# Optimization experiments

Hardware: AMD Instinct MI355X
Metric: run time of the kernel (lower is better)

## Reference

```python
import jax, jax.numpy as jnp
import numpy as np


def _mlp(h, weights, biases, n_relu):
    # Linear(+ReLU) stack; ReLU on the first n_relu layers, final layer linear only.
    for i, (w, b) in enumerate(zip(weights, biases)):
        h = h @ w + b
        if i < n_relu:
            h = jax.nn.relu(h)
    return h


def setup_inputs() -> dict:
    key = jax.random.key(0)
    ks = jax.random.split(key, 12)
    B, M, E = 16384, 512, 1024

    def lin(k, fan_in, fan_out):
        # xavier-ish scaling so activations stay well-conditioned
        return jax.random.normal(k, (fan_in, fan_out), jnp.float32) * (1.0 / np.sqrt(fan_in))

    return {
        "x": jax.random.normal(ks[0], (B, M), jnp.float32),
        "rand_noise": jax.random.uniform(ks[1], (B, M), jnp.float32),
        "u_random": jax.random.uniform(ks[2], (B, M), jnp.float32),
        "marginals_min": jnp.zeros((M,), jnp.float32),
        "marginals_max": jnp.ones((M,), jnp.float32),
        "enc_w0": lin(ks[3], M, E), "enc_b0": jnp.full((E,), 0.01, jnp.float32),
        "enc_w1": lin(ks[4], E, E), "enc_b1": jnp.full((E,), 0.01, jnp.float32),
        "enc_w2": lin(ks[5], E, E), "enc_b2": jnp.full((E,), 0.01, jnp.float32),
        "enc_w3": lin(ks[6], E, E), "enc_b3": jnp.full((E,), 0.01, jnp.float32),
        "head_w0": lin(ks[7], E, E), "head_b0": jnp.full((E,), 0.01, jnp.float32),
        "head_w1": lin(ks[8], E, E), "head_b1": jnp.full((E,), 0.01, jnp.float32),
        "corruption_len": 307,
    }


def reference(x, rand_noise, u_random, marginals_min, marginals_max,
              enc_w0, enc_b0, enc_w1, enc_b1, enc_w2, enc_b2, enc_w3, enc_b3,
              head_w0, head_b0, head_w1, head_b1, corruption_len):
    B, M = x.shape
    # Vectorized equivalent of per-row randperm(m)[:corruption_len]:
    # top-k of iid uniform noise picks a uniform random subset of size k per row.
    _, idx = jax.lax.top_k(rand_noise, corruption_len)            # [B, k]
    mask = jnp.zeros((B, M), bool).at[jnp.arange(B)[:, None], idx].set(True)

    # Marginal samples ~ Uniform(min, max) per feature.
    x_random = marginals_min + u_random * (marginals_max - marginals_min)
    x_corrupted = jnp.where(mask, x_random, x)

    enc_ws = [enc_w0, enc_w1, enc_w2, enc_w3]
    enc_bs = [enc_b0, enc_b1, enc_b2, enc_b3]
    head_ws = [head_w0, head_w1]
    head_bs = [head_b0, head_b1]

    # Run both branches through one batched pass (same math, fewer launches).
    both = jnp.concatenate([x, x_corrupted], axis=0)              # [2B, M]
    h = _mlp(both, enc_ws, enc_bs, n_relu=3)                      # encoder depth 4
    h = _mlp(h, head_ws, head_bs, n_relu=1)                       # head depth 2
    embeddings, embeddings_corrupted = h[:B], h[B:]
    return embeddings, embeddings_corrupted
```

## Files before the change

### kernel.cpp

```cpp
#include <hip/hip_runtime.h>

typedef _Float16 f16x8 __attribute__((ext_vector_type(8)));
typedef float f32x4 __attribute__((ext_vector_type(4)));

__device__ __forceinline__ void gload16(const void* g, void* l) {
  __builtin_amdgcn_global_load_lds(
      (const __attribute__((address_space(1))) void*)g,
      (__attribute__((address_space(3))) void*)l, 16, 0, 0);
}

__device__ __forceinline__ void barfence() {
  asm volatile("" ::: "memory");
  __builtin_amdgcn_s_barrier();
  asm volatile("" ::: "memory");
}

__device__ __forceinline__ int xcd_swz(int orig, int nwg) {
  int q = nwg >> 3, r = nwg & 7;
  int x = orig & 7, loc = orig >> 3;
  int base = (x < r) ? x * (q + 1) : r * (q + 1) + (x - r) * q;
  return base + loc;
}

__global__ __launch_bounds__(256) void transpose_w(const float* __restrict__ W,
                                                   _Float16* __restrict__ WT, int K) {
  const int N = 1024;
  __shared__ float tile[32][33];
  int tx = threadIdx.x, ty = threadIdx.y;
  int n0 = blockIdx.x * 32, k0 = blockIdx.y * 32;
#pragma unroll
  for (int i = 0; i < 4; i++)
    tile[ty + i * 8][tx] = W[(long)(k0 + ty + i * 8) * N + (n0 + tx)];
  __syncthreads();
#pragma unroll
  for (int i = 0; i < 4; i++)
    WT[(long)(n0 + ty + i * 8) * K + (k0 + tx)] = (_Float16)tile[tx][ty + i * 8];
}

__global__ __launch_bounds__(256) void cast_f16(const float* __restrict__ in,
                                                _Float16* __restrict__ out, long n) {
  long i = ((long)blockIdx.x * 256 + threadIdx.x) * 4;
  if (i < n) {
    float4 v = *(const float4*)(in + i);
    typedef _Float16 f16x4 __attribute__((ext_vector_type(4)));
    f16x4 o = {(_Float16)v.x, (_Float16)v.y, (_Float16)v.z, (_Float16)v.w};
    *(f16x4*)(out + i) = o;
  }
}

__global__ __launch_bounds__(256) void topk_corrupt(
    const float* __restrict__ noise, const float* __restrict__ x,
    const float* __restrict__ u, const float* __restrict__ mmin,
    const float* __restrict__ mmax, const int* __restrict__ kptr,
    _Float16* __restrict__ dplain, _Float16* __restrict__ dcorr,
    int xrow0, int nrows) {
  int lane = threadIdx.x & 63;
  int r = (blockIdx.x << 2) + (threadIdx.x >> 6);
  if (r >= nrows) return;
  long row = (long)xrow0 + r;
  long rb = row * 512 + lane * 8;
  float4 n0 = *(const float4*)(noise + rb);
  float4 n1 = *(const float4*)(noise + rb + 4);
  unsigned v[8] = {__float_as_uint(n0.x), __float_as_uint(n0.y),
                   __float_as_uint(n0.z), __float_as_uint(n0.w),
                   __float_as_uint(n1.x), __float_as_uint(n1.y),
                   __float_as_uint(n1.z), __float_as_uint(n1.w)};
  int kk = *kptr;
  unsigned T = 0;
  for (int bit = 30; bit >= 0; --bit) {
    unsigned Tp = T | (1u << bit);
    int c = 0;
#pragma unroll
    for (int j = 0; j < 8; j++) c += (int)__popcll(__ballot(v[j] >= Tp));
    if (c >= kk) T = Tp;
  }
  int cgt = 0;
  unsigned long long eqb[8];
#pragma unroll
  for (int j = 0; j < 8; j++) {
    cgt += (int)__popcll(__ballot(v[j] > T));
    eqb[j] = __ballot(v[j] == T);
  }
  int need = kk - cgt;
  unsigned long long below = (1ull << lane) - 1ull;
  int rank_base = 0;
#pragma unroll
  for (int j = 0; j < 8; j++) rank_base += (int)__popcll(eqb[j] & below);

  float4 x0 = *(const float4*)(x + rb);
  float4 x1 = *(const float4*)(x + rb + 4);
  float4 u0 = *(const float4*)(u + rb);
  float4 u1 = *(const float4*)(u + rb + 4);
  int col = lane * 8;
  float4 mn0 = *(const float4*)(mmin + col);
  float4 mn1 = *(const float4*)(mmin + col + 4);
  float4 mx0 = *(const float4*)(mmax + col);
  float4 mx1 = *(const float4*)(mmax + col + 4);
  float xs[8] = {x0.x, x0.y, x0.z, x0.w, x1.x, x1.y, x1.z, x1.w};
  float us[8] = {u0.x, u0.y, u0.z, u0.w, u1.x, u1.y, u1.z, u1.w};
  float mns[8] = {mn0.x, mn0.y, mn0.z, mn0.w, mn1.x, mn1.y, mn1.z, mn1.w};
  float mxs[8] = {mx0.x, mx0.y, mx0.z, mx0.w, mx1.x, mx1.y, mx1.z, mx1.w};

  f16x8 po, co;
  int loc = 0;
#pragma unroll
  for (int j = 0; j < 8; j++) {
    bool eq = (v[j] == T);
    int rank = rank_base + loc;
    bool m = (v[j] > T) || (eq && (rank < need));
    loc += eq ? 1 : 0;
    float rv = mns[j] + us[j] * (mxs[j] - mns[j]);
    float cv = m ? rv : xs[j];
    po[j] = (_Float16)xs[j];
    co[j] = (_Float16)cv;
  }
  long ob = (long)r * 512 + lane * 8;
  if (dplain) *(f16x8*)(dplain + ob) = po;
  *(f16x8*)(dcorr + ob) = co;
}

template <bool RELU, bool OUTF32>
__global__ __launch_bounds__(512, 2) void gemm8p(const _Float16* __restrict__ A,
                                                 const _Float16* __restrict__ BT,
                                                 const float* __restrict__ bias,
                                                 void* __restrict__ Cout, int K) {
  const int N = 1024;
  __shared__ _Float16 S[2][4][8192];
  int tid = threadIdx.x;
  int lane = tid & 63, wave = tid >> 6;
  int wr = wave >> 2, wc = wave & 3;
  int logical = xcd_swz(blockIdx.x, gridDim.x);
  long arow0 = (long)(logical >> 2) * 256;
  int bcol0 = (logical & 3) * 256;

  int srow = tid >> 3;
  int scg = (tid & 7) ^ (srow & 7);
  const _Float16* gA[2][2];
  const _Float16* gB[2][2];
#pragma unroll
  for (int h = 0; h < 2; h++)
#pragma unroll
    for (int j = 0; j < 2; j++) {
      gA[h][j] = A + (arow0 + h * 128 + j * 64 + srow) * (long)K + scg * 8;
      gB[h][j] = BT + (long)(bcol0 + h * 128 + j * 64 + srow) * K + scg * 8;
    }
  int lo = tid * 8;

#define STG_A(BUF, H, T)                                   \
  do {                                                     \
    gload16(gA[H][0] + (T) * 64, &S[BUF][H][lo]);          \
    gload16(gA[H][1] + (T) * 64, &S[BUF][H][4096 + lo]);   \
  } while (0)
#define STG_B(BUF, H, T)                                      \
  do {                                                        \
    gload16(gB[H][0] + (T) * 64, &S[BUF][2 + H][lo]);         \
    gload16(gB[H][1] + (T) * 64, &S[BUF][2 + H][4096 + lo]);  \
  } while (0)

  int lr = lane & 15, g = lane >> 4, e = lr & 7;
  int cs0 = ((0 * 4 + g) ^ e) * 8;
  int cs1 = ((1 * 4 + g) ^ e) * 8;
  int aoff[4], boff[2];
#pragma unroll
  for (int mf = 0; mf < 4; mf++) aoff[mf] = (wr * 64 + mf * 16 + lr) * 64;
#pragma unroll
  for (int nf = 0; nf < 2; nf++) boff[nf] = (wc * 32 + nf * 16 + lr) * 64;

  f16x8 af[4][2];
  f16x8 bf[2][2][2];
  f32x4 acc[2][2][4][2] = {};

#define LDA(BUF, MQ)                                                 \
  do {                                                               \
    _Pragma("unroll") for (int mf = 0; mf < 4; mf++) {               \
      af[mf][0] = *(const f16x8*)&S[BUF][MQ][aoff[mf] + cs0];        \
      af[mf][1] = *(const f16x8*)&S[BUF][MQ][aoff[mf] + cs1];        \
    }                                                                \
  } while (0)
#define LDB(BUF, NQ)                                                 \
  do {                                                               \
    _Pragma("unroll") for (int nf = 0; nf < 2; nf++) {               \
      bf[NQ][nf][0] = *(const f16x8*)&S[BUF][2 + NQ][boff[nf] + cs0];\
      bf[NQ][nf][1] = *(const f16x8*)&S[BUF][2 + NQ][boff[nf] + cs1];\
    }                                                                \
  } while (0)
#define MFMA_Q(MQ, NQ)                                               \
  do {                                                               \
    __builtin_amdgcn_s_setprio(1);                                   \
    _Pragma("unroll") for (int mf = 0; mf < 4; mf++)                 \
    _Pragma("unroll") for (int nf = 0; nf < 2; nf++)                 \
    _Pragma("unroll") for (int kk = 0; kk < 2; kk++)                 \
      acc[MQ][NQ][mf][nf] = __builtin_amdgcn_mfma_f32_16x16x32_f16(  \
          af[mf][kk], bf[NQ][nf][kk], acc[MQ][NQ][mf][nf], 0, 0, 0); \
    __builtin_amdgcn_s_setprio(0);                                   \
  } while (0)

  int NT = K / 64;
  STG_A(0, 0, 0); STG_B(0, 0, 0); STG_A(0, 1, 0); STG_B(0, 1, 0);
  if (NT > 1) {
    STG_A(1, 0, 1); STG_B(1, 0, 1);
    asm volatile("s_waitcnt vmcnt(4)" ::: "memory");
  } else {
    asm volatile("s_waitcnt vmcnt(0)" ::: "memory");
  }
  barfence();

  for (int t = 0; t < NT; ++t) {
    int buf = t & 1, nbuf = buf ^ 1;
    LDB(buf, 0);
    LDA(buf, 0);
    if (t + 1 < NT) { STG_A(nbuf, 1, t + 1); STG_B(nbuf, 1, t + 1); }
    MFMA_Q(0, 0);
    barfence();
    LDB(buf, 1);
    if (t + 2 < NT) STG_A(buf, 0, t + 2);
    MFMA_Q(0, 1);
    barfence();
    LDA(buf, 1);
    if (t + 2 < NT) STG_B(buf, 0, t + 2);
    MFMA_Q(1, 0);
    barfence();
    if (t + 1 < NT) {
      if (t + 2 < NT) asm volatile("s_waitcnt vmcnt(4)" ::: "memory");
      else            asm volatile("s_waitcnt vmcnt(0)" ::: "memory");
    }
    MFMA_Q(1, 1);
    if (t + 1 < NT) barfence();
  }
#undef STG_A
#undef STG_B
#undef LDA
#undef LDB
#undef MFMA_Q

  int r0 = (lane >> 4) * 4;
  float bv[2][2];
#pragma unroll
  for (int nq = 0; nq < 2; nq++)
#pragma unroll
    for (int nf = 0; nf < 2; nf++)
      bv[nq][nf] = bias[bcol0 + nq * 128 + wc * 32 + nf * 16 + lr];
#pragma unroll
  for (int mq = 0; mq < 2; mq++)
#pragma unroll
    for (int mf = 0; mf < 4; mf++) {
      long rowb = arow0 + mq * 128 + wr * 64 + mf * 16 + r0;
#pragma unroll
      for (int nq = 0; nq < 2; nq++)
#pragma unroll
        for (int nf = 0; nf < 2; nf++) {
          int col = bcol0 + nq * 128 + wc * 32 + nf * 16 + lr;
#pragma unroll
          for (int rr = 0; rr < 4; rr++) {
            float v = acc[mq][nq][mf][nf][rr] + bv[nq][nf];
            if (RELU) v = fmaxf(v, 0.f);
            if (OUTF32) ((float*)Cout)[(rowb + rr) * N + col] = v;
            else ((_Float16*)Cout)[(rowb + rr) * N + col] = (_Float16)v;
          }
        }
    }
}

extern "C" void kernel_launch(void* const* d_in, const int* in_sizes, int n_in,
                              void* d_out, int out_size, void* d_ws, size_t ws_size,
                              hipStream_t stream) {
  const float* x    = (const float*)d_in[0];
  const float* rn   = (const float*)d_in[1];
  const float* ur   = (const float*)d_in[2];
  const float* mmin = (const float*)d_in[3];
  const float* mmax = (const float*)d_in[4];
  const float* W[6]  = {(const float*)d_in[5],  (const float*)d_in[7],  (const float*)d_in[9],
                        (const float*)d_in[11], (const float*)d_in[13], (const float*)d_in[15]};
  const float* Bi[6] = {(const float*)d_in[6],  (const float*)d_in[8],  (const float*)d_in[10],
                        (const float*)d_in[12], (const float*)d_in[14], (const float*)d_in[16]};
  const int* kptr = (const int*)d_in[17];
  float* out = (float*)d_out;

  const long B = 16384;
  const int E = 1024;
  const int Ks[6] = {512, 1024, 1024, 1024, 1024, 1024};

  char* ws = (char*)d_ws;
  _Float16* wT[6];
  size_t off = 0;
  for (int i = 0; i < 6; i++) { wT[i] = (_Float16*)(ws + off); off += (size_t)Ks[i] * E * 2; }
  size_t rem = (ws_size > off) ? ws_size - off : 0;
  long R = 32768;
  while (R > 256 && (size_t)R * 5120 > rem) R >>= 1;

  _Float16* bothc = (_Float16*)(ws + off);
  _Float16* h0 = bothc + R * 512;
  _Float16* h1 = h0 + R * 1024;

  for (int i = 0; i < 6; i++) {
    dim3 g(E / 32, Ks[i] / 32), b(32, 8);
    transpose_w<<<g, b, 0, stream>>>(W[i], wT[i], Ks[i]);
  }

  for (long r0 = 0; r0 < 2 * B; r0 += R) {
    if (R == 2 * B) {
      topk_corrupt<<<dim3((unsigned)(B / 4)), dim3(256), 0, stream>>>(
          rn, x, ur, mmin, mmax, kptr, bothc, bothc + B * 512, 0, (int)B);
    } else {
      long plainEnd = (r0 < B) ? ((r0 + R < B) ? (r0 + R) : B) : r0;
      long p1 = plainEnd - r0;
      if (p1 > 0) {
        long n = p1 * 512;
        long blocks = (n / 4 + 255) / 256;
        cast_f16<<<dim3((unsigned)blocks), dim3(256), 0, stream>>>(x + r0 * 512, bothc, n);
      }
      long c0 = (r0 > B) ? r0 : B;
      long p2 = (r0 + R) - c0;
      if (p2 > 0) {
        topk_corrupt<<<dim3((unsigned)((p2 + 3) / 4)), dim3(256), 0, stream>>>(
            rn, x, ur, mmin, mmax, kptr, (_Float16*)nullptr,
            bothc + (c0 - r0) * 512, (int)(c0 - B), (int)p2);
      }
    }
    dim3 gg((unsigned)((R / 256) * 4)), gb(512);
    gemm8p<true,  false><<<gg, gb, 0, stream>>>(bothc, wT[0], Bi[0], (void*)h0, 512);
    gemm8p<true,  false><<<gg, gb, 0, stream>>>(h0,    wT[1], Bi[1], (void*)h1, 1024);
    gemm8p<true,  false><<<gg, gb, 0, stream>>>(h1,    wT[2], Bi[2], (void*)h0, 1024);
    gemm8p<false, false><<<gg, gb, 0, stream>>>(h0,    wT[3], Bi[3], (void*)h1, 1024);
    gemm8p<true,  false><<<gg, gb, 0, stream>>>(h1,    wT[4], Bi[4], (void*)h0, 1024);
    gemm8p<false, true ><<<gg, gb, 0, stream>>>(h0,    wT[5], Bi[5],
                                                 (void*)(out + r0 * 1024), 1024);
  }
}
```

Before: 413.5 us.

## Switch GEMM to 32x32x16 MFMA and merge weight transposes into one launch

The GEMM inner loop now uses 32x32x16 f16 MFMA tiles instead of 16x16x32, with new LDS fragment addressing, swizzle offsets and epilogue row mapping. Larger MFMA tiles reuse each loaded fragment across more output elements, which cuts LDS reads and instruction issue per FLOP. The six per-layer weight transpose kernels are also merged into a single launch that decodes the layer from blockIdx.y, saving launch overhead. The larger accumulator vectors change register pressure and the output store pattern, which risks spills or less coalesced writes.

```diff
diff --git a/kernel.cpp b/kernel.cpp
--- a/kernel.cpp
+++ b/kernel.cpp
@@ -2,6 +2,7 @@
 
 typedef _Float16 f16x8 __attribute__((ext_vector_type(8)));
 typedef float f32x4 __attribute__((ext_vector_type(4)));
+typedef float f32x16 __attribute__((ext_vector_type(16)));
 
 __device__ __forceinline__ void gload16(const void* g, void* l) {
   __builtin_amdgcn_global_load_lds(
@@ -22,12 +23,18 @@
   return base + loc;
 }
 
-__global__ __launch_bounds__(256) void transpose_w(const float* __restrict__ W,
-                                                   _Float16* __restrict__ WT, int K) {
+struct WPtrs { const float* w[6]; _Float16* wt[6]; };
+__global__ __launch_bounds__(256) void transpose_all(WPtrs p) {
   const int N = 1024;
   __shared__ float tile[32][33];
+  int y = blockIdx.y, layer, ky;
+  if (y < 16) { layer = 0; ky = y; }
+  else { int t = y - 16; layer = 1 + (t >> 5); ky = t & 31; }
+  int K = (layer == 0) ? 512 : 1024;
+  const float* W = p.w[layer];
+  _Float16* WT = p.wt[layer];
   int tx = threadIdx.x, ty = threadIdx.y;
-  int n0 = blockIdx.x * 32, k0 = blockIdx.y * 32;
+  int n0 = blockIdx.x * 32, k0 = ky * 32;
 #pragma unroll
   for (int i = 0; i < 4; i++)
     tile[ty + i * 8][tx] = W[(long)(k0 + ty + i * 8) * N + (n0 + tx)];
@@ -157,41 +164,37 @@
     gload16(gB[H][1] + (T) * 64, &S[BUF][2 + H][4096 + lo]);  \
   } while (0)
 
-  int lr = lane & 15, g = lane >> 4, e = lr & 7;
-  int cs0 = ((0 * 4 + g) ^ e) * 8;
-  int cs1 = ((1 * 4 + g) ^ e) * 8;
-  int aoff[4], boff[2];
-#pragma unroll
-  for (int mf = 0; mf < 4; mf++) aoff[mf] = (wr * 64 + mf * 16 + lr) * 64;
-#pragma unroll
-  for (int nf = 0; nf < 2; nf++) boff[nf] = (wc * 32 + nf * 16 + lr) * 64;
-
-  f16x8 af[4][2];
-  f16x8 bf[2][2][2];
-  f32x4 acc[2][2][4][2] = {};
+  int l31 = lane & 31, hi = lane >> 5, e2 = l31 & 7;
+  int acs[4];
+#pragma unroll
+  for (int kk = 0; kk < 4; kk++) acs[kk] = ((kk * 2 + hi) ^ e2) * 8;
+  int aoff2[2];
+#pragma unroll
+  for (int mb = 0; mb < 2; mb++) aoff2[mb] = (wr * 64 + mb * 32 + l31) * 64;
+  int boff2 = (wc * 32 + l31) * 64;
+
+  f16x8 af[2][4];
+  f16x8 bf[2][4];
+  f32x16 acc[2][2][2] = {};
 
 #define LDA(BUF, MQ)                                                 \
   do {                                                               \
-    _Pragma("unroll") for (int mf = 0; mf < 4; mf++) {               \
-      af[mf][0] = *(const f16x8*)&S[BUF][MQ][aoff[mf] + cs0];        \
-      af[mf][1] = *(const f16x8*)&S[BUF][MQ][aoff[mf] + cs1];        \
-    }                                                                \
+    _Pragma("unroll") for (int mb = 0; mb < 2; mb++)                 \
+    _Pragma("unroll") for (int kk = 0; kk < 4; kk++)                 \
+      af[mb][kk] = *(const f16x8*)&S[BUF][MQ][aoff2[mb] + acs[kk]];  \
   } while (0)
 #define LDB(BUF, NQ)                                                 \
   do {                                                               \
-    _Pragma("unroll") for (int nf = 0; nf < 2; nf++) {               \
-      bf[NQ][nf][0] = *(const f16x8*)&S[BUF][2 + NQ][boff[nf] + cs0];\
-      bf[NQ][nf][1] = *(const f16x8*)&S[BUF][2 + NQ][boff[nf] + cs1];\
-    }                                                                \
+    _Pragma("unroll") for (int kk = 0; kk < 4; kk++)                 \
+      bf[NQ][kk] = *(const f16x8*)&S[BUF][2 + NQ][boff2 + acs[kk]];  \
   } while (0)
 #define MFMA_Q(MQ, NQ)                                               \
   do {                                                               \
     __builtin_amdgcn_s_setprio(1);                                   \
-    _Pragma("unroll") for (int mf = 0; mf < 4; mf++)                 \
-    _Pragma("unroll") for (int nf = 0; nf < 2; nf++)                 \
-    _Pragma("unroll") for (int kk = 0; kk < 2; kk++)                 \
-      acc[MQ][NQ][mf][nf] = __builtin_amdgcn_mfma_f32_16x16x32_f16(  \
-          af[mf][kk], bf[NQ][nf][kk], acc[MQ][NQ][mf][nf], 0, 0, 0); \
+    _Pragma("unroll") for (int kk = 0; kk < 4; kk++)                 \
+    _Pragma("unroll") for (int mb = 0; mb < 2; mb++)                 \
+      acc[MQ][NQ][mb] = __builtin_amdgcn_mfma_f32_32x32x16_f16(      \
+          af[mb][kk], bf[NQ][kk], acc[MQ][NQ][mb], 0, 0, 0);         \
     __builtin_amdgcn_s_setprio(0);                                   \
   } while (0)
 
@@ -233,31 +236,26 @@
 #undef LDB
 #undef MFMA_Q
 
-  int r0 = (lane >> 4) * 4;
-  float bv[2][2];
-#pragma unroll
-  for (int nq = 0; nq < 2; nq++)
-#pragma unroll
-    for (int nf = 0; nf < 2; nf++)
-      bv[nq][nf] = bias[bcol0 + nq * 128 + wc * 32 + nf * 16 + lr];
+  float bv2[2];
+#pragma unroll
+  for (int nq = 0; nq < 2; nq++) bv2[nq] = bias[bcol0 + nq * 128 + wc * 32 + l31];
 #pragma unroll
   for (int mq = 0; mq < 2; mq++)
 #pragma unroll
-    for (int mf = 0; mf < 4; mf++) {
-      long rowb = arow0 + mq * 128 + wr * 64 + mf * 16 + r0;
-#pragma unroll
-      for (int nq = 0; nq < 2; nq++)
-#pragma unroll
-        for (int nf = 0; nf < 2; nf++) {
-          int col = bcol0 + nq * 128 + wc * 32 + nf * 16 + lr;
-#pragma unroll
-          for (int rr = 0; rr < 4; rr++) {
-            float v = acc[mq][nq][mf][nf][rr] + bv[nq][nf];
-            if (RELU) v = fmaxf(v, 0.f);
-            if (OUTF32) ((float*)Cout)[(rowb + rr) * N + col] = v;
-            else ((_Float16*)Cout)[(rowb + rr) * N + col] = (_Float16)v;
-          }
+    for (int mb = 0; mb < 2; mb++) {
+      long rowb = arow0 + mq * 128 + wr * 64 + mb * 32 + hi * 4;
+#pragma unroll
+      for (int nq = 0; nq < 2; nq++) {
+        int col = bcol0 + nq * 128 + wc * 32 + l31;
+#pragma unroll
+        for (int rg = 0; rg < 16; rg++) {
+          long rrow = rowb + (rg & 3) + 8 * (rg >> 2);
+          float v = acc[mq][nq][mb][rg] + bv2[nq];
+          if (RELU) v = fmaxf(v, 0.f);
+          if (OUTF32) ((float*)Cout)[rrow * N + col] = v;
+          else ((_Float16*)Cout)[rrow * N + col] = (_Float16)v;
         }
+      }
     }
 }
 
@@ -292,10 +290,9 @@
   _Float16* h0 = bothc + R * 512;
   _Float16* h1 = h0 + R * 1024;
 
-  for (int i = 0; i < 6; i++) {
-    dim3 g(E / 32, Ks[i] / 32), b(32, 8);
-    transpose_w<<<g, b, 0, stream>>>(W[i], wT[i], Ks[i]);
-  }
+  WPtrs wp;
+  for (int i = 0; i < 6; i++) { wp.w[i] = W[i]; wp.wt[i] = wT[i]; }
+  transpose_all<<<dim3(E / 32, 16 + 5 * 32), dim3(32, 8), 0, stream>>>(wp);
 
   for (long r0 = 0; r0 < 2 * B; r0 += R) {
     if (R == 2 * B) {
```

New measurement: 436.6 us. +5.6%, slower.
